# Kernel tuning notes

Measured on AMD Instinct MI355X. Metric: run time of the kernel, lower is better.

Reference implementation:

```python
import jax, jax.numpy as jnp
import numpy as np
import math

EMBED_DIM = 768
HEADS = 6
HEAD_DIM = EMBED_DIM // HEADS


def setup_inputs() -> dict:
    key = jax.random.key(0)
    ks = jax.random.split(key, 9)
    B, L, D = 4, 2048, EMBED_DIM
    s = 1.0 / math.sqrt(D)
    return {
        "x_input": jax.random.normal(ks[0], (B, L, D), dtype=jnp.float32),
        "Wq": jax.random.normal(ks[1], (D, D), dtype=jnp.float32) * s,
        "bq": jnp.zeros((D,), dtype=jnp.float32),
        "Wk": jax.random.normal(ks[2], (D, D), dtype=jnp.float32) * s,
        "bk": jnp.zeros((D,), dtype=jnp.float32),
        "Wv": jax.random.normal(ks[3], (D, D), dtype=jnp.float32) * s,
        "bv": jnp.zeros((D,), dtype=jnp.float32),
        "Wo": jax.random.normal(ks[4], (D, D), dtype=jnp.float32) * s,
        "bo": jnp.zeros((D,), dtype=jnp.float32),
    }


def reference(x_input, Wq, bq, Wk, bk, Wv, bv, Wo, bo):
    B, L, D = x_input.shape
    # QKV projections
    q = x_input @ Wq + bq
    k = x_input @ Wk + bk
    v = x_input @ Wv + bv
    # [B, L, D] -> [B, H, L, hd]
    def split_heads(t):
        return t.reshape(B, L, HEADS, HEAD_DIM).transpose(0, 2, 1, 3)
    q, k, v = split_heads(q), split_heads(k), split_heads(v)
    # scaled dot-product scores [B, H, L, L]
    scores = jnp.einsum("bhqd,bhkd->bhqk", q, k) / math.sqrt(HEAD_DIM)
    # causal mask: query i attends to keys j <= i
    causal = jnp.tril(jnp.ones((L, L), dtype=bool))
    scores = jnp.where(causal, scores, jnp.finfo(scores.dtype).min)
    attn = jax.nn.softmax(scores, axis=-1)
    out = jnp.einsum("bhqk,bhkd->bhqd", attn, v)  # [B, H, L, hd]
    out = out.transpose(0, 2, 1, 3).reshape(B, L, D)
    # output projection (dropout = identity in eval mode)
    return out @ Wo + bo
```

## Files before the change

kernel.cpp:

```cpp
#include <hip/hip_runtime.h>
#include <hip/hip_bf16.h>
#include <stdint.h>

#define D_EMB 768
#define NHEADS 6
#define HD 128
#define BATCH 4
#define SEQ 2048
#define BH (BATCH*NHEADS)
#define M_ROWS (BATCH*SEQ)

typedef float f32x4 __attribute__((ext_vector_type(4)));
typedef __bf16 bf16x8 __attribute__((ext_vector_type(8)));
typedef short short8 __attribute__((ext_vector_type(8)));

__device__ __forceinline__ short f2bf(float f) {
  union { float f; uint32_t u; } x; x.f = f;
  uint32_t r = x.u + 0x7fffu + ((x.u >> 16) & 1u);
  return (short)(r >> 16);
}

__device__ __forceinline__ void gload16(const void* g, void* l) {
  __builtin_amdgcn_global_load_lds(
      (const __attribute__((address_space(1))) unsigned int*)g,
      (__attribute__((address_space(3))) unsigned int*)l, 16, 0, 0);
}

__global__ void cvt_f32_bf16_k(const float* __restrict__ in, short* __restrict__ out, int n4) {
  int i = blockIdx.x * 256 + threadIdx.x;
  if (i >= n4) return;
  float4 v = ((const float4*)in)[i];
  short4 o;
  o.x = f2bf(v.x); o.y = f2bf(v.y); o.z = f2bf(v.z); o.w = f2bf(v.w);
  ((short4*)out)[i] = o;
}

__global__ void transpose_w_k(const float* __restrict__ in, short* __restrict__ out, int R, int C) {
  __shared__ float tile[32][33];
  int c0 = blockIdx.x * 32, r0 = blockIdx.y * 32;
  int tx = threadIdx.x, ty = threadIdx.y;
  #pragma unroll
  for (int i = 0; i < 32; i += 8)
    tile[ty + i][tx] = in[(size_t)(r0 + ty + i) * C + (c0 + tx)];
  __syncthreads();
  #pragma unroll
  for (int i = 0; i < 32; i += 8)
    out[(size_t)(c0 + ty + i) * R + (r0 + tx)] = f2bf(tile[tx][ty + i]);
}

__global__ void transpose_v_k(const short* __restrict__ in, short* __restrict__ out) {
  __shared__ short tile[32][33];
  const int hidx = blockIdx.z;
  const short* src = in + (size_t)hidx * SEQ * HD;
  short* dst = out + (size_t)hidx * SEQ * HD;
  int d0 = blockIdx.x * 32;
  int l0 = blockIdx.y * 32;
  int tx = threadIdx.x, ty = threadIdx.y;
  #pragma unroll
  for (int i = 0; i < 32; i += 8)
    tile[ty + i][tx] = src[(size_t)(l0 + ty + i) * HD + d0 + tx];
  __syncthreads();
  #pragma unroll
  for (int i = 0; i < 32; i += 8)
    dst[(size_t)(d0 + ty + i) * SEQ + l0 + tx] = tile[tx][ty + i];
}

__global__ __launch_bounds__(256) void gemm_bt_k(
    const short* __restrict__ A, const short* __restrict__ BT,
    const float* __restrict__ bias,
    float* __restrict__ Cf, short* __restrict__ Cb,
    int M, int N, int K, int mode)
{
  __shared__ short Als[2][128][32];
  __shared__ short Bls[2][64][32];
  const int tid = threadIdx.x;
  const int lane = tid & 63;
  const int wave = tid >> 6;
  const int m0 = blockIdx.x * 128;
  const int n0 = blockIdx.y * 64;
  const int wm = (wave & 1) * 64;
  const int wn = (wave >> 1) * 32;
  const int lr = tid >> 2;
  const int lc = (tid & 3) * 8;
  const int frow = lane & 15;
  const int kk = (lane >> 4) * 8;

  #define G_STAGE(buf, k0)                                                      \
    do {                                                                        \
      gload16(&A[(size_t)(m0 + lr) * K + (k0) + lc],                            \
              (char*)Als[buf] + wave * 1024);                                   \
      gload16(&A[(size_t)(m0 + lr + 64) * K + (k0) + lc],                       \
              (char*)Als[buf] + 4096 + wave * 1024);                            \
      gload16(&BT[(size_t)(n0 + lr) * K + (k0) + lc],                           \
              (char*)Bls[buf] + wave * 1024);                                   \
    } while (0)

  f32x4 acc[4][2] = {};
  G_STAGE(0, 0);
  __syncthreads();
  int buf = 0;
  for (int k0 = 0; k0 < K; k0 += 32) {
    if (k0 + 32 < K) G_STAGE(buf ^ 1, k0 + 32);
    bf16x8 af[4], bfv[2];
    #pragma unroll
    for (int i = 0; i < 4; ++i)
      af[i] = *(const bf16x8*)&Als[buf][wm + i * 16 + frow][kk];
    #pragma unroll
    for (int j = 0; j < 2; ++j)
      bfv[j] = *(const bf16x8*)&Bls[buf][wn + j * 16 + frow][kk];
    #pragma unroll
    for (int i = 0; i < 4; ++i)
      #pragma unroll
      for (int j = 0; j < 2; ++j)
        acc[i][j] = __builtin_amdgcn_mfma_f32_16x16x32_bf16(af[i], bfv[j], acc[i][j], 0, 0, 0);
    __syncthreads();
    buf ^= 1;
  }
  #undef G_STAGE

  const int r0l = (lane >> 4) * 4;
  const int cl = lane & 15;
  #pragma unroll
  for (int i = 0; i < 4; ++i) {
    #pragma unroll
    for (int j = 0; j < 2; ++j) {
      int col = n0 + wn + j * 16 + cl;
      float bv = bias ? bias[col] : 0.f;
      #pragma unroll
      for (int r = 0; r < 4; ++r) {
        int m = m0 + wm + i * 16 + r0l + r;
        float v = acc[i][j][r] + bv;
        if (mode == 0) {
          Cf[(size_t)m * N + col] = v;
        } else {
          int b = m >> 11, li = m & 2047;
          int h = col >> 7, d = col & 127;
          Cb[((((size_t)b * NHEADS + h) << 11) + li) * HD + d] = f2bf(v);
        }
      }
    }
  }
}

__global__ __launch_bounds__(256, 4) void attn_causal_k(
    const short* __restrict__ Q, const short* __restrict__ K,
    const short* __restrict__ Vt, short* __restrict__ O)
{
  __shared__ short Kls[2][32 * 128];
  __shared__ short Vls[2][128 * 32];
  __shared__ short Pls[4][16 * 64];

  const int tid = threadIdx.x;
  const int lane = tid & 63;
  const int wave = tid >> 6;
  const int g = lane >> 4;
  const int cl = lane & 15;

  const int bid = (int)blockIdx.x;
  const int sid = (bid & 7) * 96 + (bid >> 3);
  const int bh = sid >> 5;
  const int qb = 31 - (sid & 31);
  const int q0 = qb * 64;
  const int qw0 = q0 + wave * 16;

  const short* Qh = Q + (size_t)bh * SEQ * HD;
  const short* Kh = K + (size_t)bh * SEQ * HD;
  const short* Vh = Vt + (size_t)bh * SEQ * HD;

  bf16x8 qf[4];
  #pragma unroll
  for (int c = 0; c < 4; ++c)
    qf[c] = *(const bf16x8*)&Qh[(size_t)(qw0 + cl) * HD + c * 32 + g * 8];

  f32x4 o[8] = {};
  float lrow[4] = {0.f, 0.f, 0.f, 0.f};

  const float kSc = 0.08838834764831845f * 1.44269504088896341f;
  const int swzr = (cl & 7) << 4;
  const int swzv = (cl & 3) << 4;
  char* Pw = (char*)&Pls[wave][0];
  const int nt = 2 * (qb + 1);

  #define STAGE(b, t)                                                            \
    do {                                                                         \
      const int j0s = (t) * 32;                                                  \
      _Pragma("unroll")                                                          \
      for (int i = 0; i < 2; ++i) {                             \
        int row = i * 16 + (tid >> 4);                                           \
        int colb = ((tid & 15) * 16) ^ ((row & 7) << 4);                         \
        gload16((const char*)Kh + (size_t)(j0s + row) * 256 + colb,              \
                (char*)Kls[b] + i * 4096 + wave * 1024);                         \
      }                                                                          \
      _Pragma("unroll")                                                          \
      for (int i = 0; i < 2; ++i) {                            \
        int row = i * 64 + (tid >> 2);                                           \
        int colb = ((tid & 3) * 16) ^ ((row & 3) << 4);                          \
        gload16((const char*)Vh + ((size_t)row * SEQ + j0s) * 2 + colb,          \
                (char*)Vls[b] + i * 4096 + wave * 1024);                         \
      }                                                                          \
    } while (0)

  STAGE(0, 0);
  int buf = 0;
  for (int t = 0; t < nt; ++t) {
    __syncthreads();
    if (t + 1 < nt) STAGE(buf ^ 1, t + 1);
    const int j0 = t * 32;

    f32x4 s[2] = {};
    #pragma unroll
    for (int jf = 0; jf < 2; ++jf)
      #pragma unroll
      for (int c = 0; c < 4; ++c) {
        bf16x8 kf = *(const bf16x8*)((const char*)Kls[buf] + (jf * 16 + cl) * 256 +
                                     ((c * 64 + g * 16) ^ swzr));
        s[jf] = __builtin_amdgcn_mfma_f32_16x16x32_bf16(qf[c], kf, s[jf], 0, 0, 0);
      }

    #pragma unroll
    for (int r = 0; r < 4; ++r) {
      const int qi = qw0 + g * 4 + r;
      const int rl = g * 4 + r;
      const int swzw = (rl & 7) << 4;
      float ps = 0.f;
      #pragma unroll
      for (int jf = 0; jf < 2; ++jf) {
        const int j = j0 + jf * 16 + cl;
        float p = (j > qi) ? 0.f : __builtin_amdgcn_exp2f(s[jf][r] * kSc);
        ps += p;
        *(short*)(Pw + rl * 128 + (((jf * 16 + cl) * 2) ^ swzw)) = f2bf(p);
      }
      lrow[r] += ps;
    }
    asm volatile("s_waitcnt lgkmcnt(0)" ::: "memory");
    __builtin_amdgcn_sched_barrier(0);

    bf16x8 pf = *(const bf16x8*)(Pw + cl * 128 + ((g * 16) ^ swzr));
    #pragma unroll
    for (int f = 0; f < 8; ++f) {
      bf16x8 vf = *(const bf16x8*)((const char*)Vls[buf] + (f * 16 + cl) * 64 +
                                   ((g * 16) ^ swzv));
      o[f] = __builtin_amdgcn_mfma_f32_16x16x32_bf16(pf, vf, o[f], 0, 0, 0);
    }
    buf ^= 1;
  }
  #undef STAGE

  #pragma unroll
  for (int r = 0; r < 4; ++r)
    #pragma unroll
    for (int off2 = 1; off2 < 16; off2 <<= 1)
      lrow[r] += __shfl_xor(lrow[r], off2);

  const int b = bh / NHEADS, h = bh % NHEADS;
  #pragma unroll
  for (int r = 0; r < 4; ++r) {
    const int qi = qw0 + g * 4 + r;
    const float invl = 1.0f / lrow[r];
    size_t base = ((size_t)b * SEQ + qi) * D_EMB + h * HD;
    #pragma unroll
    for (int f = 0; f < 8; ++f)
      O[base + f * 16 + cl] = f2bf(o[f][r] * invl);
  }
}

extern "C" void kernel_launch(void* const* d_in, const int* in_sizes, int n_in,
                              void* d_out, int out_size, void* d_ws, size_t ws_size,
                              hipStream_t stream) {
  const float* x  = (const float*)d_in[0];
  const float* Wq = (const float*)d_in[1];
  const float* bq = (const float*)d_in[2];
  const float* Wk = (const float*)d_in[3];
  const float* bk = (const float*)d_in[4];
  const float* Wv = (const float*)d_in[5];
  const float* bv = (const float*)d_in[6];
  const float* Wo = (const float*)d_in[7];
  const float* bo = (const float*)d_in[8];
  float* out = (float*)d_out;

  char* ws = (char*)d_ws;
  size_t off = 0;
  auto carve = [&](size_t bytes) {
    char* p = ws + off;
    off += (bytes + 255) & ~(size_t)255;
    return p;
  };
  short* xb  = (short*)carve((size_t)M_ROWS * D_EMB * 2);
  short* wqt = (short*)carve((size_t)D_EMB * D_EMB * 2);
  short* wkt = (short*)carve((size_t)D_EMB * D_EMB * 2);
  short* wvt = (short*)carve((size_t)D_EMB * D_EMB * 2);
  short* wot = (short*)carve((size_t)D_EMB * D_EMB * 2);
  short* Qb  = (short*)carve((size_t)BH * SEQ * HD * 2);
  short* Kb  = (short*)carve((size_t)BH * SEQ * HD * 2);
  short* Vb  = (short*)carve((size_t)BH * SEQ * HD * 2);
  short* Vtb = (short*)carve((size_t)BH * SEQ * HD * 2);
  short* Ob  = (short*)carve((size_t)M_ROWS * D_EMB * 2);

  int n4 = M_ROWS * D_EMB / 4;
  cvt_f32_bf16_k<<<(n4 + 255) / 256, 256, 0, stream>>>(x, xb, n4);

  dim3 tb(32, 8);
  transpose_w_k<<<dim3(24, 24), tb, 0, stream>>>(Wq, wqt, D_EMB, D_EMB);
  transpose_w_k<<<dim3(24, 24), tb, 0, stream>>>(Wk, wkt, D_EMB, D_EMB);
  transpose_w_k<<<dim3(24, 24), tb, 0, stream>>>(Wv, wvt, D_EMB, D_EMB);
  transpose_w_k<<<dim3(24, 24), tb, 0, stream>>>(Wo, wot, D_EMB, D_EMB);

  dim3 gg(M_ROWS / 128, D_EMB / 64);
  gemm_bt_k<<<gg, 256, 0, stream>>>(xb, wqt, bq, nullptr, Qb, M_ROWS, D_EMB, D_EMB, 1);
  gemm_bt_k<<<gg, 256, 0, stream>>>(xb, wkt, bk, nullptr, Kb, M_ROWS, D_EMB, D_EMB, 1);
  gemm_bt_k<<<gg, 256, 0, stream>>>(xb, wvt, bv, nullptr, Vb, M_ROWS, D_EMB, D_EMB, 1);

  transpose_v_k<<<dim3(HD / 32, SEQ / 32, BH), tb, 0, stream>>>(Vb, Vtb);

  attn_causal_k<<<dim3(768), 256, 0, stream>>>(Qb, Kb, Vtb, Ob);

  gemm_bt_k<<<gg, 256, 0, stream>>>(Ob, wot, bo, out, nullptr, M_ROWS, D_EMB, D_EMB, 0);
}
```

Measured before the change: 267.0 us.

## Fuse QKV projections into one GEMM and enlarge GEMM and attention tiles

The three Q/K/V projection GEMMs become one launch over a concatenated transposed weight, with the output slot and bias chosen per column tile. GEMM tiles grow from 128x64 to 128x128 so each wave computes 64x64. The attention kernel now processes 64-key blocks per iteration instead of 32, halving loop iterations and barriers, with a new V swizzle and occupancy lowered to 2 blocks per SM. This trades fewer launches and syncs and more operand reuse for higher register and LDS pressure and fewer GEMM blocks in flight.

```diff
diff --git a/kernel.cpp b/kernel.cpp
--- a/kernel.cpp
+++ b/kernel.cpp
@@ -67,51 +67,49 @@
 
 __global__ __launch_bounds__(256) void gemm_bt_k(
     const short* __restrict__ A, const short* __restrict__ BT,
-    const float* __restrict__ bias,
+    const float* __restrict__ b0, const float* __restrict__ b1, const float* __restrict__ b2,
     float* __restrict__ Cf, short* __restrict__ Cb,
     int M, int N, int K, int mode)
 {
-  __shared__ short Als[2][128][32];
-  __shared__ short Bls[2][64][32];
+  __shared__ short Als[2][128 * 32];
+  __shared__ short Bls[2][128 * 32];
   const int tid = threadIdx.x;
   const int lane = tid & 63;
   const int wave = tid >> 6;
   const int m0 = blockIdx.x * 128;
-  const int n0 = blockIdx.y * 64;
+  const int n0 = blockIdx.y * 128;
   const int wm = (wave & 1) * 64;
-  const int wn = (wave >> 1) * 32;
-  const int lr = tid >> 2;
-  const int lc = (tid & 3) * 8;
+  const int wn = (wave >> 1) * 64;
   const int frow = lane & 15;
   const int kk = (lane >> 4) * 8;
 
-  #define G_STAGE(buf, k0)                                                      \
-    do {                                                                        \
-      gload16(&A[(size_t)(m0 + lr) * K + (k0) + lc],                            \
-              (char*)Als[buf] + wave * 1024);                                   \
-      gload16(&A[(size_t)(m0 + lr + 64) * K + (k0) + lc],                       \
-              (char*)Als[buf] + 4096 + wave * 1024);                            \
-      gload16(&BT[(size_t)(n0 + lr) * K + (k0) + lc],                           \
-              (char*)Bls[buf] + wave * 1024);                                   \
+  #define G_STAGE(buf, k0)                                                       \
+    do {                                                                         \
+      _Pragma("unroll")                                                          \
+      for (int i = 0; i < 2; ++i) {                                              \
+        gload16(&A[(size_t)(m0 + i * 64 + (tid >> 2)) * K + (k0) + (tid & 3) * 8], \
+                (char*)Als[buf] + i * 4096 + wave * 1024);                       \
+        gload16(&BT[(size_t)(n0 + i * 64 + (tid >> 2)) * K + (k0) + (tid & 3) * 8], \
+                (char*)Bls[buf] + i * 4096 + wave * 1024);                       \
+      }                                                                          \
     } while (0)
 
-  f32x4 acc[4][2] = {};
+  f32x4 acc[4][4] = {};
   G_STAGE(0, 0);
   __syncthreads();
   int buf = 0;
   for (int k0 = 0; k0 < K; k0 += 32) {
     if (k0 + 32 < K) G_STAGE(buf ^ 1, k0 + 32);
-    bf16x8 af[4], bfv[2];
+    bf16x8 af[4], bfv[4];
+    #pragma unroll
+    for (int i = 0; i < 4; ++i) {
+      af[i]  = *(const bf16x8*)((const char*)Als[buf] + (wm + i * 16 + frow) * 64 + kk * 2);
+      bfv[i] = *(const bf16x8*)((const char*)Bls[buf] + (wn + i * 16 + frow) * 64 + kk * 2);
+    }
     #pragma unroll
     for (int i = 0; i < 4; ++i)
-      af[i] = *(const bf16x8*)&Als[buf][wm + i * 16 + frow][kk];
-    #pragma unroll
-    for (int j = 0; j < 2; ++j)
-      bfv[j] = *(const bf16x8*)&Bls[buf][wn + j * 16 + frow][kk];
-    #pragma unroll
-    for (int i = 0; i < 4; ++i)
-      #pragma unroll
-      for (int j = 0; j < 2; ++j)
+      #pragma unroll
+      for (int j = 0; j < 4; ++j)
         acc[i][j] = __builtin_amdgcn_mfma_f32_16x16x32_bf16(af[i], bfv[j], acc[i][j], 0, 0, 0);
     __syncthreads();
     buf ^= 1;
@@ -120,35 +118,39 @@
 
   const int r0l = (lane >> 4) * 4;
   const int cl = lane & 15;
+  const int t3 = n0 / 768;
+  const int nloc = n0 - t3 * 768;
+  const float* bp = (t3 == 0) ? b0 : ((t3 == 1) ? b1 : b2);
+  short* Cbt = Cb + (size_t)t3 * ((size_t)BH * SEQ * HD);
   #pragma unroll
   for (int i = 0; i < 4; ++i) {
     #pragma unroll
-    for (int j = 0; j < 2; ++j) {
-      int col = n0 + wn + j * 16 + cl;
-      float bv = bias ? bias[col] : 0.f;
+    for (int j = 0; j < 4; ++j) {
+      int coll = nloc + wn + j * 16 + cl;
+      float bv = bp[coll];
       #pragma unroll
       for (int r = 0; r < 4; ++r) {
         int m = m0 + wm + i * 16 + r0l + r;
         float v = acc[i][j][r] + bv;
         if (mode == 0) {
-          Cf[(size_t)m * N + col] = v;
+          Cf[(size_t)m * N + (n0 + wn + j * 16 + cl)] = v;
         } else {
           int b = m >> 11, li = m & 2047;
-          int h = col >> 7, d = col & 127;
-          Cb[((((size_t)b * NHEADS + h) << 11) + li) * HD + d] = f2bf(v);
+          int h = coll >> 7, d = coll & 127;
+          Cbt[((((size_t)b * NHEADS + h) << 11) + li) * HD + d] = f2bf(v);
         }
       }
     }
   }
 }
 
-__global__ __launch_bounds__(256, 4) void attn_causal_k(
+__global__ __launch_bounds__(256, 2) void attn_causal_k(
     const short* __restrict__ Q, const short* __restrict__ K,
     const short* __restrict__ Vt, short* __restrict__ O)
 {
-  __shared__ short Kls[2][32 * 128];
-  __shared__ short Vls[2][128 * 32];
-  __shared__ short Pls[4][16 * 64];
+  __shared__ __attribute__((aligned(16))) short Kls[2][64 * 128];
+  __shared__ __attribute__((aligned(16))) short Vls[2][128 * 64];
+  __shared__ __attribute__((aligned(16))) short Pls[4][16 * 64];
 
   const int tid = threadIdx.x;
   const int lane = tid & 63;
@@ -177,24 +179,23 @@
 
   const float kSc = 0.08838834764831845f * 1.44269504088896341f;
   const int swzr = (cl & 7) << 4;
-  const int swzv = (cl & 3) << 4;
   char* Pw = (char*)&Pls[wave][0];
-  const int nt = 2 * (qb + 1);
+  const int nt = qb + 1;
 
   #define STAGE(b, t)                                                            \
     do {                                                                         \
-      const int j0s = (t) * 32;                                                  \
+      const int j0s = (t) * 64;                                                  \
       _Pragma("unroll")                                                          \
-      for (int i = 0; i < 2; ++i) {                             \
-        int row = i * 16 + (tid >> 4);                                           \
-        int colb = ((tid & 15) * 16) ^ ((row & 7) << 4);                         \
+      for (int i = 0; i < 4; ++i) {                  \
+        int row = i * 16 + wave * 4 + (lane >> 4);                               \
+        int colb = ((lane & 15) * 16) ^ ((row & 7) << 4);                        \
         gload16((const char*)Kh + (size_t)(j0s + row) * 256 + colb,              \
                 (char*)Kls[b] + i * 4096 + wave * 1024);                         \
       }                                                                          \
       _Pragma("unroll")                                                          \
-      for (int i = 0; i < 2; ++i) {                            \
-        int row = i * 64 + (tid >> 2);                                           \
-        int colb = ((tid & 3) * 16) ^ ((row & 3) << 4);                          \
+      for (int i = 0; i < 4; ++i) {                 \
+        int row = i * 32 + wave * 8 + (lane >> 3);                               \
+        int colb = ((lane & 7) * 16) ^ ((row & 7) << 4);                         \
         gload16((const char*)Vh + ((size_t)row * SEQ + j0s) * 2 + colb,          \
                 (char*)Vls[b] + i * 4096 + wave * 1024);                         \
       }                                                                          \
@@ -205,11 +206,11 @@
   for (int t = 0; t < nt; ++t) {
     __syncthreads();
     if (t + 1 < nt) STAGE(buf ^ 1, t + 1);
-    const int j0 = t * 32;
-
-    f32x4 s[2] = {};
-    #pragma unroll
-    for (int jf = 0; jf < 2; ++jf)
+    const int j0 = t * 64;
+
+    f32x4 s[4] = {};
+    #pragma unroll
+    for (int jf = 0; jf < 4; ++jf)
       #pragma unroll
       for (int c = 0; c < 4; ++c) {
         bf16x8 kf = *(const bf16x8*)((const char*)Kls[buf] + (jf * 16 + cl) * 256 +
@@ -224,7 +225,7 @@
       const int swzw = (rl & 7) << 4;
       float ps = 0.f;
       #pragma unroll
-      for (int jf = 0; jf < 2; ++jf) {
+      for (int jf = 0; jf < 4; ++jf) {
         const int j = j0 + jf * 16 + cl;
         float p = (j > qi) ? 0.f : __builtin_amdgcn_exp2f(s[jf][r] * kSc);
         ps += p;
@@ -235,12 +236,15 @@
     asm volatile("s_waitcnt lgkmcnt(0)" ::: "memory");
     __builtin_amdgcn_sched_barrier(0);
 
-    bf16x8 pf = *(const bf16x8*)(Pw + cl * 128 + ((g * 16) ^ swzr));
-    #pragma unroll
-    for (int f = 0; f < 8; ++f) {
-      bf16x8 vf = *(const bf16x8*)((const char*)Vls[buf] + (f * 16 + cl) * 64 +
-                                   ((g * 16) ^ swzv));
-      o[f] = __builtin_amdgcn_mfma_f32_16x16x32_bf16(pf, vf, o[f], 0, 0, 0);
+    #pragma unroll
+    for (int ks = 0; ks < 2; ++ks) {
+      bf16x8 pf = *(const bf16x8*)(Pw + cl * 128 + ((ks * 64 + g * 16) ^ swzr));
+      #pragma unroll
+      for (int f = 0; f < 8; ++f) {
+        bf16x8 vf = *(const bf16x8*)((const char*)Vls[buf] + (f * 16 + cl) * 128 +
+                                     ((ks * 64 + g * 16) ^ swzr));
+        o[f] = __builtin_amdgcn_mfma_f32_16x16x32_bf16(pf, vf, o[f], 0, 0, 0);
+      }
     }
     buf ^= 1;
   }
@@ -285,34 +289,32 @@
     off += (bytes + 255) & ~(size_t)255;
     return p;
   };
-  short* xb  = (short*)carve((size_t)M_ROWS * D_EMB * 2);
-  short* wqt = (short*)carve((size_t)D_EMB * D_EMB * 2);
-  short* wkt = (short*)carve((size_t)D_EMB * D_EMB * 2);
-  short* wvt = (short*)carve((size_t)D_EMB * D_EMB * 2);
-  short* wot = (short*)carve((size_t)D_EMB * D_EMB * 2);
+  short* xb     = (short*)carve((size_t)M_ROWS * D_EMB * 2);
+  short* wqkvT  = (short*)carve((size_t)3 * D_EMB * D_EMB * 2);
+  short* wot    = (short*)carve((size_t)D_EMB * D_EMB * 2);
   short* Qb  = (short*)carve((size_t)BH * SEQ * HD * 2);
   short* Kb  = (short*)carve((size_t)BH * SEQ * HD * 2);
   short* Vb  = (short*)carve((size_t)BH * SEQ * HD * 2);
   short* Vtb = (short*)carve((size_t)BH * SEQ * HD * 2);
   short* Ob  = (short*)carve((size_t)M_ROWS * D_EMB * 2);
+  (void)Kb; (void)Vb;
 
   int n4 = M_ROWS * D_EMB / 4;
   cvt_f32_bf16_k<<<(n4 + 255) / 256, 256, 0, stream>>>(x, xb, n4);
 
   dim3 tb(32, 8);
-  transpose_w_k<<<dim3(24, 24), tb, 0, stream>>>(Wq, wqt, D_EMB, D_EMB);
-  transpose_w_k<<<dim3(24, 24), tb, 0, stream>>>(Wk, wkt, D_EMB, D_EMB);
-  transpose_w_k<<<dim3(24, 24), tb, 0, stream>>>(Wv, wvt, D_EMB, D_EMB);
+  transpose_w_k<<<dim3(24, 24), tb, 0, stream>>>(Wq, wqkvT,                 D_EMB, D_EMB);
+  transpose_w_k<<<dim3(24, 24), tb, 0, stream>>>(Wk, wqkvT +     D_EMB*D_EMB, D_EMB, D_EMB);
+  transpose_w_k<<<dim3(24, 24), tb, 0, stream>>>(Wv, wqkvT + 2 * D_EMB*D_EMB, D_EMB, D_EMB);
   transpose_w_k<<<dim3(24, 24), tb, 0, stream>>>(Wo, wot, D_EMB, D_EMB);
 
-  dim3 gg(M_ROWS / 128, D_EMB / 64);
-  gemm_bt_k<<<gg, 256, 0, stream>>>(xb, wqt, bq, nullptr, Qb, M_ROWS, D_EMB, D_EMB, 1);
-  gemm_bt_k<<<gg, 256, 0, stream>>>(xb, wkt, bk, nullptr, Kb, M_ROWS, D_EMB, D_EMB, 1);
-  gemm_bt_k<<<gg, 256, 0, stream>>>(xb, wvt, bv, nullptr, Vb, M_ROWS, D_EMB, D_EMB, 1);
+  gemm_bt_k<<<dim3(M_ROWS / 128, (3 * D_EMB) / 128), 256, 0, stream>>>(
+      xb, wqkvT, bq, bk, bv, nullptr, Qb, M_ROWS, 3 * D_EMB, D_EMB, 1);
 
   transpose_v_k<<<dim3(HD / 32, SEQ / 32, BH), tb, 0, stream>>>(Vb, Vtb);
 
   attn_causal_k<<<dim3(768), 256, 0, stream>>>(Qb, Kb, Vtb, Ob);
 
-  gemm_bt_k<<<gg, 256, 0, stream>>>(Ob, wot, bo, out, nullptr, M_ROWS, D_EMB, D_EMB, 0);
-}
+  gemm_bt_k<<<dim3(M_ROWS / 128, D_EMB / 128), 256, 0, stream>>>(
+      Ob, wot, bo, bo, bo, out, nullptr, M_ROWS, D_EMB, D_EMB, 0);
+}
```

Measured after the change: 239.2 us. 1.12x faster.
